# Kernel optimization log

Measured on AMD Instinct MI355X. Metric: run time of the kernel, lower is better.

The kernel has to match this reference:

```python
import jax, jax.numpy as jnp
import numpy as np

B, F, D, A = 1024, 33, 128, 128  # batch, num_fields, embed_dim, attn_size (A must equal gnn dim)

def setup_inputs() -> dict:
    key = jax.random.key(0)
    k1, k2, k3, k4 = jax.random.split(key, 4)
    gnn_feature = jax.random.normal(k1, (B, A), dtype=jnp.float32)
    x = jax.random.normal(k2, (B, F, D), dtype=jnp.float32)
    # attention Linear(embed_dim -> attn_size): weight (A, D), bias (A,)
    lim = 1.0 / np.sqrt(D)
    attn_W = jax.random.uniform(k3, (A, D), minval=-lim, maxval=lim, dtype=jnp.float32)
    attn_b = jax.random.uniform(k4, (A,), minval=-lim, maxval=lim, dtype=jnp.float32)
    return {"gnn_feature": gnn_feature, "x": x, "attn_W": attn_W, "attn_b": attn_b}

def reference(gnn_feature, x, attn_W, attn_b):
    num_fields = x.shape[1]
    row, col = np.triu_indices(num_fields, k=1)  # P = F*(F-1)/2 pairs
    inner = x[:, row] * x[:, col]                # [B, P, D]
    fm = jax.nn.relu(jnp.einsum('bpd,ad->bpa', inner, attn_W) + attn_b)  # [B, P, A]
    # bmm(gnn[b,1,A], fm[b,p,A,1]) -> dot product per pair, softmax over pairs
    scores = jnp.einsum('ba,bpa->bp', gnn_feature, fm)  # [B, P]
    attn = jax.nn.softmax(scores, axis=1)               # [B, P]
    attn_output = jnp.einsum('bp,bpd->bd', attn, inner) * 100.0  # [B, D]
    return jnp.concatenate([gnn_feature, attn_output], axis=1)   # [B, A+D]
```

## Files before the change

### kernel.cpp

```cpp
#include <hip/hip_runtime.h>

#define FN 33
#define DN 128
#define AN 128
#define PN 528
#define XS 136
#define TS 36

typedef __attribute__((ext_vector_type(8))) _Float16 half8;
typedef __attribute__((ext_vector_type(4))) float f32x4;
typedef __attribute__((ext_vector_type(4))) unsigned int u32x4;

__device__ __forceinline__ unsigned int pkrtz(float a, float b) {
  return __builtin_bit_cast(unsigned int, __builtin_amdgcn_cvt_pkrtz(a, b));
}

__device__ __forceinline__ float row_sum16(float v) {
  v += __builtin_bit_cast(float, __builtin_amdgcn_update_dpp(0, __builtin_bit_cast(int, v), 0x128, 0xF, 0xF, false));
  v += __builtin_bit_cast(float, __builtin_amdgcn_update_dpp(0, __builtin_bit_cast(int, v), 0x124, 0xF, 0xF, false));
  v += __builtin_bit_cast(float, __builtin_amdgcn_update_dpp(0, __builtin_bit_cast(int, v), 0x122, 0xF, 0xF, false));
  v += __builtin_bit_cast(float, __builtin_amdgcn_update_dpp(0, __builtin_bit_cast(int, v), 0x121, 0xF, 0xF, false));
  return v;
}

#define WALK(XHB, GB, SPB)                                                    \
  {                                                                           \
    const int t_beg = mh ? 17 : 0;                                            \
    const int t_end = mh ? 33 : 17;                                           \
    unsigned int rc_next = rowcol[t_beg * 16 + u];                            \
    for (int t = t_beg; t < t_end; ++t) {                                     \
      const unsigned int rc = rc_next;                                        \
      if (t + 1 < t_end) rc_next = rowcol[(t + 1) * 16 + u];                  \
      const int r = rc & 255, c = rc >> 8;                                    \
      const _Float16* xr_base = &XHB[r * XS + q * 8];                         \
      const _Float16* xc_base = &XHB[c * XS + q * 8];                         \
      f32x4 acc[4];                                                           \
      _Pragma("unroll")                                                       \
      for (int nn = 0; nn < 4; nn++) acc[nn] = (f32x4){0.f, 0.f, 0.f, 0.f};   \
      __builtin_amdgcn_s_setprio(1);                                          \
      _Pragma("unroll")                                                       \
      for (int kk = 0; kk < 4; kk++) {                                        \
        half8 af = *(const half8*)(xr_base + kk * 32) *                       \
                   *(const half8*)(xc_base + kk * 32);                        \
        _Pragma("unroll")                                                     \
        for (int nn = 0; nn < 4; nn++)                                        \
          acc[nn] = __builtin_amdgcn_mfma_f32_16x16x32_f16(af, Bf[nn][kk],    \
                                                           acc[nn], 0, 0, 0);  \
      }                                                                       \
      __builtin_amdgcn_s_setprio(0);                                          \
      float sc[4] = {0.f, 0.f, 0.f, 0.f};                                     \
      _Pragma("unroll")                                                       \
      for (int nn = 0; nn < 4; nn++)                                          \
        _Pragma("unroll")                                                     \
        for (int rr = 0; rr < 4; rr++)                                        \
          sc[rr] = fmaf(fmaxf(acc[nn][rr] + barr[nn], 0.f), GB[nn], sc[rr]);  \
      _Pragma("unroll")                                                       \
      for (int rr = 0; rr < 4; rr++) sc[rr] = row_sum16(sc[rr]);              \
      if (u == 0)                                                             \
        *(f32x4*)&SPB[t * 16 + q * 4] = (f32x4){sc[0], sc[1], sc[2], sc[3]};  \
    }                                                                         \
  }

#define EPI(A2D, XHB)                                                         \
  {                                                                           \
    const int d = tid & 127;                                                  \
    const int h = tid >> 7;                                                   \
    float xcol[36];                                                           \
    _Pragma("unroll")                                                         \
    for (int i = 0; i < FN; i++) xcol[i] = (float)XHB[i * XS + d];            \
    xcol[33] = 0.f; xcol[34] = 0.f; xcol[35] = 0.f;                           \
    float accv = 0.f;                                                         \
    _Pragma("unroll")                                                         \
    for (int i = 0; i < 32; i++) {                                            \
      if ((i & 1) != h) continue;                                             \
      const int L = FN - 1 - i;                                               \
      const int nf4 = (L + 3) >> 2;                                           \
      float ti = 0.f;                                                         \
      _Pragma("unroll")                                                       \
      for (int t = 0; t < nf4; t++) {                                         \
        f32x4 a4 = *(const f32x4*)&A2D[i * TS + t * 4];                       \
        ti = fmaf(a4.x, xcol[i + 1 + t * 4 + 0], ti);                         \
        ti = fmaf(a4.y, xcol[i + 1 + t * 4 + 1], ti);                         \
        ti = fmaf(a4.z, xcol[i + 1 + t * 4 + 2], ti);                         \
        ti = fmaf(a4.w, xcol[i + 1 + t * 4 + 3], ti);                         \
      }                                                                       \
      accv = fmaf(xcol[i], ti, accv);                                         \
    }                                                                         \
    part[tid] = accv;                                                         \
  }

__global__ __launch_bounds__(256, 2)
void afm_kernel(const float* __restrict__ gnn, const float* __restrict__ xg,
                const float* __restrict__ Wg,  const float* __restrict__ bg,
                float* __restrict__ out)
{
  __shared__ __align__(16) _Float16 xh[2][FN * XS];
  __shared__ __align__(16) float attn2d[2][FN * TS];
  __shared__ __align__(16) float sp[2][2][PN];
  __shared__ __align__(16) float part[256];
  __shared__ unsigned short rowcol[PN];
  __shared__ float red[16];

  const int tid  = threadIdx.x;
  const int b0   = blockIdx.x * 2;
  const int b1   = b0 + 1;
  const int wave = tid >> 6;
  const int lane = tid & 63;
  const int q    = lane >> 4;
  const int u    = lane & 15;
  const int nh   = wave & 1;
  const int mh   = wave >> 1;

  const f32x4* xb0 = (const f32x4*)(xg + (size_t)b0 * FN * DN);
  const f32x4* xb1 = (const f32x4*)(xg + (size_t)b1 * FN * DN);
  f32x4 xv0[4], xv1[4], xt0 = {0,0,0,0}, xt1 = {0,0,0,0};
  #pragma unroll
  for (int s = 0; s < 4; s++) xv0[s] = xb0[tid + s * 256];
  #pragma unroll
  for (int s = 0; s < 4; s++) xv1[s] = xb1[tid + s * 256];
  const bool tail = tid < 32;
  if (tail) { xt0 = xb0[1024 + tid]; xt1 = xb1[1024 + tid]; }

  half8 Bf[4][4];
  float g0[4], g1[4], barr[4];
  #pragma unroll
  for (int nn = 0; nn < 4; nn++) {
    const int a = nh * 64 + nn * 16 + u;
    const float* src = Wg + (size_t)a * DN + q * 8;
    #pragma unroll
    for (int kk = 0; kk < 4; kk++) {
      f32x4 w0 = *(const f32x4*)(src + kk * 32);
      f32x4 w1 = *(const f32x4*)(src + kk * 32 + 4);
      u32x4 pk;
      pk.x = pkrtz(w0.x, w0.y);
      pk.y = pkrtz(w0.z, w0.w);
      pk.z = pkrtz(w1.x, w1.y);
      pk.w = pkrtz(w1.z, w1.w);
      Bf[nn][kk] = __builtin_bit_cast(half8, pk);
      asm volatile("" : "+v"(Bf[nn][kk]));
    }
    g0[nn] = gnn[(size_t)b0 * AN + a];
    g1[nn] = gnn[(size_t)b1 * AN + a];
    barr[nn] = bg[a];
    asm volatile("" : "+v"(g0[nn]), "+v"(g1[nn]), "+v"(barr[nn]));
  }

  {
    float* a2z = &attn2d[0][0];
    for (int idx = tid; idx < 2 * FN * TS; idx += 256) a2z[idx] = 0.0f;
    for (int p = tid; p < PN; p += 256) {
      int i = 0, rem = p;
      while (rem >= FN - 1 - i) { rem -= FN - 1 - i; i++; }
      rowcol[p] = (unsigned short)(i | ((i + 1 + rem) << 8));
    }
  }

  #pragma unroll
  for (int s = 0; s < 4; s++) {
    const int idx = tid + s * 256;
    const int i = idx >> 5, d0 = (idx & 31) << 2;
    *(uint2*)&xh[0][i * XS + d0] = make_uint2(pkrtz(xv0[s].x, xv0[s].y), pkrtz(xv0[s].z, xv0[s].w));
    *(uint2*)&xh[1][i * XS + d0] = make_uint2(pkrtz(xv1[s].x, xv1[s].y), pkrtz(xv1[s].z, xv1[s].w));
  }
  if (tail) {
    const int idx = 1024 + tid;
    const int i = idx >> 5, d0 = (idx & 31) << 2;
    *(uint2*)&xh[0][i * XS + d0] = make_uint2(pkrtz(xt0.x, xt0.y), pkrtz(xt0.z, xt0.w));
    *(uint2*)&xh[1][i * XS + d0] = make_uint2(pkrtz(xt1.x, xt1.y), pkrtz(xt1.z, xt1.w));
  }
  __syncthreads();

  WALK(xh[0], g0, (&sp[0][nh][0]));
  __syncthreads();

  float s0a = sp[0][0][tid] + sp[0][1][tid];
  float s1a = sp[0][0][tid + 256] + sp[0][1][tid + 256];
  float s2a = (tid < 16) ? (sp[0][0][tid + 512] + sp[0][1][tid + 512]) : -3.4e38f;
  {
    float m = fmaxf(fmaxf(s0a, s1a), s2a);
    #pragma unroll
    for (int off = 32; off >= 1; off >>= 1) m = fmaxf(m, __shfl_xor(m, off, 64));
    if (lane == 0) red[wave] = m;
  }
  __syncthreads();

  const float smax0 = fmaxf(fmaxf(red[0], red[1]), fmaxf(red[2], red[3]));
  {
    float e0 = __expf(s0a - smax0);
    float e1 = __expf(s1a - smax0);
    float e2 = (tid < 16) ? __expf(s2a - smax0) : 0.f;
    unsigned int rc = rowcol[tid];
    attn2d[0][(rc & 255) * TS + ((rc >> 8) - (rc & 255) - 1)] = e0;
    rc = rowcol[tid + 256];
    attn2d[0][(rc & 255) * TS + ((rc >> 8) - (rc & 255) - 1)] = e1;
    if (tid < 16) {
      rc = rowcol[tid + 512];
      attn2d[0][(rc & 255) * TS + ((rc >> 8) - (rc & 255) - 1)] = e2;
    }
    float lsum = e0 + e1 + e2;
    #pragma unroll
    for (int off = 32; off >= 1; off >>= 1) lsum += __shfl_xor(lsum, off, 64);
    if (lane == 0) red[4 + wave] = lsum;
  }
  __syncthreads();
  const float Z0 = (red[4] + red[5]) + (red[6] + red[7]);

  WALK(xh[1], g1, (&sp[1][nh][0]));
  EPI(attn2d[0], xh[0]);
  __syncthreads();

  float s0b = sp[1][0][tid] + sp[1][1][tid];
  float s1b = sp[1][0][tid + 256] + sp[1][1][tid + 256];
  float s2b = (tid < 16) ? (sp[1][0][tid + 512] + sp[1][1][tid + 512]) : -3.4e38f;
  {
    float m = fmaxf(fmaxf(s0b, s1b), s2b);
    #pragma unroll
    for (int off = 32; off >= 1; off >>= 1) m = fmaxf(m, __shfl_xor(m, off, 64));
    if (lane == 0) red[8 + wave] = m;
  }
  if (tid < DN) {
    float tot = part[tid] + part[tid + 128];
    out[(size_t)b0 * (AN + DN) + AN + tid] = tot * (100.0f / Z0);
  } else {
    const int a = tid - 128;
    out[(size_t)b0 * (AN + DN) + a] = gnn[(size_t)b0 * AN + a];
  }
  __syncthreads();

  const float smax1 = fmaxf(fmaxf(red[8], red[9]), fmaxf(red[10], red[11]));
  {
    float e0 = __expf(s0b - smax1);
    float e1 = __expf(s1b - smax1);
    float e2 = (tid < 16) ? __expf(s2b - smax1) : 0.f;
    unsigned int rc = rowcol[tid];
    attn2d[1][(rc & 255) * TS + ((rc >> 8) - (rc & 255) - 1)] = e0;
    rc = rowcol[tid + 256];
    attn2d[1][(rc & 255) * TS + ((rc >> 8) - (rc & 255) - 1)] = e1;
    if (tid < 16) {
      rc = rowcol[tid + 512];
      attn2d[1][(rc & 255) * TS + ((rc >> 8) - (rc & 255) - 1)] = e2;
    }
    float lsum = e0 + e1 + e2;
    #pragma unroll
    for (int off = 32; off >= 1; off >>= 1) lsum += __shfl_xor(lsum, off, 64);
    if (lane == 0) red[12 + wave] = lsum;
  }
  __syncthreads();
  const float Z1 = (red[12] + red[13]) + (red[14] + red[15]);

  EPI(attn2d[1], xh[1]);
  __syncthreads();

  if (tid < DN) {
    float tot = part[tid] + part[tid + 128];
    out[(size_t)b1 * (AN + DN) + AN + tid] = tot * (100.0f / Z1);
  } else {
    const int a = tid - 128;
    out[(size_t)b1 * (AN + DN) + a] = gnn[(size_t)b1 * AN + a];
  }
}

extern "C" void kernel_launch(void* const* d_in, const int* in_sizes, int n_in,
                              void* d_out, int out_size, void* d_ws, size_t ws_size,
                              hipStream_t stream) {
  (void)n_in; (void)out_size; (void)d_ws; (void)ws_size;
  const float* gnn  = (const float*)d_in[0];
  const float* x    = (const float*)d_in[1];
  const float* W    = (const float*)d_in[2];
  const float* bias = (const float*)d_in[3];
  float* out = (float*)d_out;
  const int Bn = in_sizes[0] / AN;
  afm_kernel<<<dim3(Bn / 2), dim3(256), 0, stream>>>(gnn, x, W, bias, out);
}
```

Measured before the change: 106.9 us.

## Process four batches per block with a software pipeline and fused softmax max

```diff
diff --git a/kernel.cpp b/kernel.cpp
--- a/kernel.cpp
+++ b/kernel.cpp
@@ -23,10 +23,40 @@
   return v;
 }
 
-#define WALK(XHB, GB, SPB)                                                    \
+#define XLOAD(XV, XT, BB)                                                     \
+  {                                                                           \
+    const f32x4* xb = (const f32x4*)(xg + (size_t)(BB) * FN * DN);            \
+    _Pragma("unroll")                                                         \
+    for (int s = 0; s < 4; s++) {                                             \
+      XV[s] = xb[tid + s * 256];                                              \
+      asm volatile("" : "+v"(XV[s]));                                         \
+    }                                                                         \
+    if (tid < 32) XT = xb[1024 + tid];                                        \
+    asm volatile("" : "+v"(XT));                                              \
+  }
+
+#define XSTORE(XV, XT, BUFI)                                                  \
+  {                                                                           \
+    _Pragma("unroll")                                                         \
+    for (int s = 0; s < 4; s++) {                                             \
+      const int idx = tid + s * 256;                                          \
+      const int i = idx >> 5, d0 = (idx & 31) << 2;                           \
+      *(uint2*)&xh[BUFI][i * XS + d0] =                                       \
+          make_uint2(pkrtz(XV[s].x, XV[s].y), pkrtz(XV[s].z, XV[s].w));       \
+    }                                                                         \
+    if (tid < 32) {                                                           \
+      const int idx = 1024 + tid;                                             \
+      const int i = idx >> 5, d0 = (idx & 31) << 2;                           \
+      *(uint2*)&xh[BUFI][i * XS + d0] =                                       \
+          make_uint2(pkrtz(XT.x, XT.y), pkrtz(XT.z, XT.w));                   \
+    }                                                                         \
+  }
+
+#define WALK(XHB, GB, SPB, RMAXP)                                             \
   {                                                                           \
     const int t_beg = mh ? 17 : 0;                                            \
     const int t_end = mh ? 33 : 17;                                           \
+    float wm = -3.4e38f;                                                      \
     unsigned int rc_next = rowcol[t_beg * 16 + u];                            \
     for (int t = t_beg; t < t_end; ++t) {                                     \
       const unsigned int rc = rc_next;                                        \
@@ -56,15 +86,45 @@
           sc[rr] = fmaf(fmaxf(acc[nn][rr] + barr[nn], 0.f), GB[nn], sc[rr]);  \
       _Pragma("unroll")                                                       \
       for (int rr = 0; rr < 4; rr++) sc[rr] = row_sum16(sc[rr]);              \
+      wm = fmaxf(wm, fmaxf(fmaxf(sc[0], sc[1]), fmaxf(sc[2], sc[3])));        \
       if (u == 0)                                                             \
         *(f32x4*)&SPB[t * 16 + q * 4] = (f32x4){sc[0], sc[1], sc[2], sc[3]};  \
     }                                                                         \
-  }
-
-#define EPI(A2D, XHB)                                                         \
-  {                                                                           \
-    const int d = tid & 127;                                                  \
-    const int h = tid >> 7;                                                   \
+    wm = fmaxf(wm, __shfl_xor(wm, 16, 64));                                   \
+    wm = fmaxf(wm, __shfl_xor(wm, 32, 64));                                   \
+    if (lane == 0) RMAXP[wave] = wm;                                          \
+  }
+
+#define SPH(PARM)                                                             \
+  {                                                                           \
+    const float Mh = fmaxf(rmax[PARM][0], rmax[PARM][2]) +                    \
+                     fmaxf(rmax[PARM][1], rmax[PARM][3]);                     \
+    float s0 = sp[PARM][0][tid] + sp[PARM][1][tid];                           \
+    float s1 = sp[PARM][0][tid + 256] + sp[PARM][1][tid + 256];               \
+    float e0 = __expf(s0 - Mh);                                               \
+    float e1 = __expf(s1 - Mh);                                               \
+    unsigned int rc = rowcol[tid];                                            \
+    attn2d[PARM][(rc & 255) * TS + ((rc >> 8) - (rc & 255) - 1)] = e0;        \
+    rc = rowcol[tid + 256];                                                   \
+    attn2d[PARM][(rc & 255) * TS + ((rc >> 8) - (rc & 255) - 1)] = e1;        \
+    float e2 = 0.f;                                                           \
+    if (tid < 16) {                                                           \
+      float s2 = sp[PARM][0][tid + 512] + sp[PARM][1][tid + 512];             \
+      e2 = __expf(s2 - Mh);                                                   \
+      rc = rowcol[tid + 512];                                                 \
+      attn2d[PARM][(rc & 255) * TS + ((rc >> 8) - (rc & 255) - 1)] = e2;      \
+    }                                                                         \
+    float ls = (e0 + e1) + e2;                                                \
+    _Pragma("unroll")                                                         \
+    for (int off = 32; off >= 1; off >>= 1) ls += __shfl_xor(ls, off, 64);    \
+    if (lane == 0) rsum[PARM][wave] = ls;                                     \
+  }
+
+#define EPH(PARM, XHB, BB)                                                    \
+  if (tid < 128) {                                                            \
+    const float Zb = (rsum[PARM][0] + rsum[PARM][1]) +                        \
+                     (rsum[PARM][2] + rsum[PARM][3]);                         \
+    const int d = tid;                                                        \
     float xcol[36];                                                           \
     _Pragma("unroll")                                                         \
     for (int i = 0; i < FN; i++) xcol[i] = (float)XHB[i * XS + d];            \
@@ -72,13 +132,12 @@
     float accv = 0.f;                                                         \
     _Pragma("unroll")                                                         \
     for (int i = 0; i < 32; i++) {                                            \
-      if ((i & 1) != h) continue;                                             \
       const int L = FN - 1 - i;                                               \
       const int nf4 = (L + 3) >> 2;                                           \
       float ti = 0.f;                                                         \
       _Pragma("unroll")                                                       \
       for (int t = 0; t < nf4; t++) {                                         \
-        f32x4 a4 = *(const f32x4*)&A2D[i * TS + t * 4];                       \
+        f32x4 a4 = *(const f32x4*)&attn2d[PARM][i * TS + t * 4];              \
         ti = fmaf(a4.x, xcol[i + 1 + t * 4 + 0], ti);                         \
         ti = fmaf(a4.y, xcol[i + 1 + t * 4 + 1], ti);                         \
         ti = fmaf(a4.z, xcol[i + 1 + t * 4 + 2], ti);                         \
@@ -86,24 +145,25 @@
       }                                                                       \
       accv = fmaf(xcol[i], ti, accv);                                         \
     }                                                                         \
-    part[tid] = accv;                                                         \
-  }
-
-__global__ __launch_bounds__(256, 2)
+    out[(size_t)(BB) * (AN + DN) + AN + d] = accv * (100.0f / Zb);            \
+  } else {                                                                    \
+    const int a = tid - 128;                                                  \
+    out[(size_t)(BB) * (AN + DN) + a] = gnn[(size_t)(BB) * AN + a];           \
+  }
+
+__global__ __launch_bounds__(256, 1)
 void afm_kernel(const float* __restrict__ gnn, const float* __restrict__ xg,
                 const float* __restrict__ Wg,  const float* __restrict__ bg,
                 float* __restrict__ out)
 {
-  __shared__ __align__(16) _Float16 xh[2][FN * XS];
+  __shared__ __align__(16) _Float16 xh[4][FN * XS];
   __shared__ __align__(16) float attn2d[2][FN * TS];
   __shared__ __align__(16) float sp[2][2][PN];
-  __shared__ __align__(16) float part[256];
   __shared__ unsigned short rowcol[PN];
-  __shared__ float red[16];
+  __shared__ float rmax[2][4], rsum[2][4];
 
   const int tid  = threadIdx.x;
-  const int b0   = blockIdx.x * 2;
-  const int b1   = b0 + 1;
+  const int b0   = blockIdx.x * 4;
   const int wave = tid >> 6;
   const int lane = tid & 63;
   const int q    = lane >> 4;
@@ -111,18 +171,13 @@
   const int nh   = wave & 1;
   const int mh   = wave >> 1;
 
-  const f32x4* xb0 = (const f32x4*)(xg + (size_t)b0 * FN * DN);
-  const f32x4* xb1 = (const f32x4*)(xg + (size_t)b1 * FN * DN);
-  f32x4 xv0[4], xv1[4], xt0 = {0,0,0,0}, xt1 = {0,0,0,0};
-  #pragma unroll
-  for (int s = 0; s < 4; s++) xv0[s] = xb0[tid + s * 256];
-  #pragma unroll
-  for (int s = 0; s < 4; s++) xv1[s] = xb1[tid + s * 256];
-  const bool tail = tid < 32;
-  if (tail) { xt0 = xb0[1024 + tid]; xt1 = xb1[1024 + tid]; }
+  f32x4 xv0[4], xv1[4];
+  f32x4 xt0 = {0,0,0,0}, xt1 = {0,0,0,0};
+  XLOAD(xv0, xt0, b0 + 0);
+  XLOAD(xv1, xt1, b0 + 1);
 
   half8 Bf[4][4];
-  float g0[4], g1[4], barr[4];
+  float g[4][4], barr[4];
   #pragma unroll
   for (int nn = 0; nn < 4; nn++) {
     const int a = nh * 64 + nn * 16 + u;
@@ -139,10 +194,13 @@
       Bf[nn][kk] = __builtin_bit_cast(half8, pk);
       asm volatile("" : "+v"(Bf[nn][kk]));
     }
-    g0[nn] = gnn[(size_t)b0 * AN + a];
-    g1[nn] = gnn[(size_t)b1 * AN + a];
+    #pragma unroll
+    for (int bi = 0; bi < 4; bi++) {
+      g[bi][nn] = gnn[(size_t)(b0 + bi) * AN + a];
+      asm volatile("" : "+v"(g[bi][nn]));
+    }
     barr[nn] = bg[a];
-    asm volatile("" : "+v"(g0[nn]), "+v"(g1[nn]), "+v"(barr[nn]));
+    asm volatile("" : "+v"(barr[nn]));
   }
 
   {
@@ -154,110 +212,42 @@
       rowcol[p] = (unsigned short)(i | ((i + 1 + rem) << 8));
     }
   }
-
-  #pragma unroll
-  for (int s = 0; s < 4; s++) {
-    const int idx = tid + s * 256;
-    const int i = idx >> 5, d0 = (idx & 31) << 2;
-    *(uint2*)&xh[0][i * XS + d0] = make_uint2(pkrtz(xv0[s].x, xv0[s].y), pkrtz(xv0[s].z, xv0[s].w));
-    *(uint2*)&xh[1][i * XS + d0] = make_uint2(pkrtz(xv1[s].x, xv1[s].y), pkrtz(xv1[s].z, xv1[s].w));
-  }
-  if (tail) {
-    const int idx = 1024 + tid;
-    const int i = idx >> 5, d0 = (idx & 31) << 2;
-    *(uint2*)&xh[0][i * XS + d0] = make_uint2(pkrtz(xt0.x, xt0.y), pkrtz(xt0.z, xt0.w));
-    *(uint2*)&xh[1][i * XS + d0] = make_uint2(pkrtz(xt1.x, xt1.y), pkrtz(xt1.z, xt1.w));
-  }
-  __syncthreads();
-
-  WALK(xh[0], g0, (&sp[0][nh][0]));
-  __syncthreads();
-
-  float s0a = sp[0][0][tid] + sp[0][1][tid];
-  float s1a = sp[0][0][tid + 256] + sp[0][1][tid + 256];
-  float s2a = (tid < 16) ? (sp[0][0][tid + 512] + sp[0][1][tid + 512]) : -3.4e38f;
+  XSTORE(xv0, xt0, 0);
+  XSTORE(xv1, xt1, 1);
+  __syncthreads();
+
   {
-    float m = fmaxf(fmaxf(s0a, s1a), s2a);
-    #pragma unroll
-    for (int off = 32; off >= 1; off >>= 1) m = fmaxf(m, __shfl_xor(m, off, 64));
-    if (lane == 0) red[wave] = m;
-  }
-  __syncthreads();
-
-  const float smax0 = fmaxf(fmaxf(red[0], red[1]), fmaxf(red[2], red[3]));
+    f32x4 xv2[4], xt2 = {0,0,0,0};
+    XLOAD(xv2, xt2, b0 + 2);
+    WALK(xh[0], g[0], (&sp[0][nh][0]), rmax[0]);
+    XSTORE(xv2, xt2, 2);
+  }
+  __syncthreads();
+
   {
-    float e0 = __expf(s0a - smax0);
-    float e1 = __expf(s1a - smax0);
-    float e2 = (tid < 16) ? __expf(s2a - smax0) : 0.f;
-    unsigned int rc = rowcol[tid];
-    attn2d[0][(rc & 255) * TS + ((rc >> 8) - (rc & 255) - 1)] = e0;
-    rc = rowcol[tid + 256];
-    attn2d[0][(rc & 255) * TS + ((rc >> 8) - (rc & 255) - 1)] = e1;
-    if (tid < 16) {
-      rc = rowcol[tid + 512];
-      attn2d[0][(rc & 255) * TS + ((rc >> 8) - (rc & 255) - 1)] = e2;
-    }
-    float lsum = e0 + e1 + e2;
-    #pragma unroll
-    for (int off = 32; off >= 1; off >>= 1) lsum += __shfl_xor(lsum, off, 64);
-    if (lane == 0) red[4 + wave] = lsum;
-  }
-  __syncthreads();
-  const float Z0 = (red[4] + red[5]) + (red[6] + red[7]);
-
-  WALK(xh[1], g1, (&sp[1][nh][0]));
-  EPI(attn2d[0], xh[0]);
-  __syncthreads();
-
-  float s0b = sp[1][0][tid] + sp[1][1][tid];
-  float s1b = sp[1][0][tid + 256] + sp[1][1][tid + 256];
-  float s2b = (tid < 16) ? (sp[1][0][tid + 512] + sp[1][1][tid + 512]) : -3.4e38f;
-  {
-    float m = fmaxf(fmaxf(s0b, s1b), s2b);
-    #pragma unroll
-    for (int off = 32; off >= 1; off >>= 1) m = fmaxf(m, __shfl_xor(m, off, 64));
-    if (lane == 0) red[8 + wave] = m;
-  }
-  if (tid < DN) {
-    float tot = part[tid] + part[tid + 128];
-    out[(size_t)b0 * (AN + DN) + AN + tid] = tot * (100.0f / Z0);
-  } else {
-    const int a = tid - 128;
-    out[(size_t)b0 * (AN + DN) + a] = gnn[(size_t)b0 * AN + a];
-  }
-  __syncthreads();
-
-  const float smax1 = fmaxf(fmaxf(red[8], red[9]), fmaxf(red[10], red[11]));
-  {
-    float e0 = __expf(s0b - smax1);
-    float e1 = __expf(s1b - smax1);
-    float e2 = (tid < 16) ? __expf(s2b - smax1) : 0.f;
-    unsigned int rc = rowcol[tid];
-    attn2d[1][(rc & 255) * TS + ((rc >> 8) - (rc & 255) - 1)] = e0;
-    rc = rowcol[tid + 256];
-    attn2d[1][(rc & 255) * TS + ((rc >> 8) - (rc & 255) - 1)] = e1;
-    if (tid < 16) {
-      rc = rowcol[tid + 512];
-      attn2d[1][(rc & 255) * TS + ((rc >> 8) - (rc & 255) - 1)] = e2;
-    }
-    float lsum = e0 + e1 + e2;
-    #pragma unroll
-    for (int off = 32; off >= 1; off >>= 1) lsum += __shfl_xor(lsum, off, 64);
-    if (lane == 0) red[12 + wave] = lsum;
-  }
-  __syncthreads();
-  const float Z1 = (red[12] + red[13]) + (red[14] + red[15]);
-
-  EPI(attn2d[1], xh[1]);
-  __syncthreads();
-
-  if (tid < DN) {
-    float tot = part[tid] + part[tid + 128];
-    out[(size_t)b1 * (AN + DN) + AN + tid] = tot * (100.0f / Z1);
-  } else {
-    const int a = tid - 128;
-    out[(size_t)b1 * (AN + DN) + a] = gnn[(size_t)b1 * AN + a];
-  }
+    f32x4 xv3[4], xt3 = {0,0,0,0};
+    XLOAD(xv3, xt3, b0 + 3);
+    WALK(xh[1], g[1], (&sp[1][nh][0]), rmax[1]);
+    SPH(0);
+    XSTORE(xv3, xt3, 3);
+  }
+  __syncthreads();
+
+  WALK(xh[2], g[2], (&sp[0][nh][0]), rmax[0]);
+  SPH(1);
+  EPH(0, xh[0], b0 + 0);
+  __syncthreads();
+
+  WALK(xh[3], g[3], (&sp[1][nh][0]), rmax[1]);
+  SPH(0);
+  EPH(1, xh[1], b0 + 1);
+  __syncthreads();
+
+  SPH(1);
+  EPH(0, xh[2], b0 + 2);
+  __syncthreads();
+
+  EPH(1, xh[3], b0 + 3);
 }
 
 extern "C" void kernel_launch(void* const* d_in, const int* in_sizes, int n_in,
@@ -270,5 +260,5 @@
   const float* bias = (const float*)d_in[3];
   float* out = (float*)d_out;
   const int Bn = in_sizes[0] / AN;
-  afm_kernel<<<dim3(Bn / 2), dim3(256), 0, stream>>>(gnn, x, W, bias, out);
-}
+  afm_kernel<<<dim3(Bn / 4), dim3(256), 0, stream>>>(gnn, x, W, bias, out);
+}
```

Result: slower. 129.9 us (+21.5%).
